# Kernel tuning notes

Measured on AMD Instinct MI355X. Metric: run time of the kernel, lower is better.

Reference implementation:

```python
import jax, jax.numpy as jnp
import numpy as np

NUM_HEADS = 32
NUM_KV_HEADS = 8
HEAD_DIM = 128
SCALE = 0.08838834764831845  # 1/sqrt(HEAD_DIM)
SEQ_LEN = 2048
NEG_INF = -1e30


def setup_inputs() -> dict:
    key = jax.random.key(0)
    k1, k2, k3 = jax.random.split(key, 3)
    query = jax.random.normal(k1, (SEQ_LEN, NUM_HEADS * HEAD_DIM), dtype=jnp.float32)
    key_t = jax.random.normal(k2, (SEQ_LEN, NUM_KV_HEADS * HEAD_DIM), dtype=jnp.float32)
    value = jax.random.normal(k3, (SEQ_LEN, NUM_KV_HEADS * HEAD_DIM), dtype=jnp.float32)
    return {"query": query, "key": key_t, "value": value}


def reference(query, key, value):
    S = query.shape[0]
    n_rep = NUM_HEADS // NUM_KV_HEADS
    # GQA: group q heads by kv head instead of materializing repeated K/V.
    q = query.reshape(S, NUM_KV_HEADS, n_rep, HEAD_DIM)   # [S, G, R, D]
    k = key.reshape(S, NUM_KV_HEADS, HEAD_DIM)            # [S, G, D]
    v = value.reshape(S, NUM_KV_HEADS, HEAD_DIM)          # [S, G, D]
    # scores: [G, R, S(query), S(key)]
    scores = jnp.einsum('sgrd,tgd->grst', q, k) * jnp.float32(SCALE)
    # causal mask (prefill: seq_len > 1 -> is_causal=True)
    causal = jnp.arange(S)[:, None] >= jnp.arange(S)[None, :]  # [S, S]
    scores = jnp.where(causal, scores, NEG_INF)
    probs = jax.nn.softmax(scores, axis=-1)
    out = jnp.einsum('grst,tgd->sgrd', probs, v)          # [S, G, R, D]
    return out.reshape(S, NUM_HEADS * HEAD_DIM)
```

## Files before the change

kernel.cpp:

```cpp
#include <hip/hip_runtime.h>


#define SEQ    2048
#define NH     32
#define NKV    8
#define DHEAD  128
#define QROW   (NH * DHEAD)
#define KVROW  (NKV * DHEAD)
#define SCALE  0.08838834764831845f
#define LOG2E  1.4426950408889634f
#define BN     64
#define VSTRP  132

typedef __attribute__((ext_vector_type(8))) short bf16x8;
typedef __attribute__((ext_vector_type(8))) unsigned short u16x8;
typedef __attribute__((ext_vector_type(16))) float f32x16;
typedef __attribute__((ext_vector_type(4))) unsigned int u32x4;

static __device__ __forceinline__ unsigned short f2bf(float f) {
  unsigned int u = __float_as_uint(f);
  return (unsigned short)((u + 0x7fffu + ((u >> 16) & 1u)) >> 16);
}

static __device__ __forceinline__ unsigned cvtpk_bf16(float lo, float hi) {
  unsigned r;
  asm("v_cvt_pk_bf16_f32 %0, %1, %2" : "=v"(r) : "v"(lo), "v"(hi));
  return r;
}

static __device__ __forceinline__ f32x16 zero16() {
  f32x16 z;
#pragma unroll
  for (int i = 0; i < 16; ++i) z[i] = 0.f;
  return z;
}

__global__ __launch_bounds__(256) void prep_kernel(
    const float* __restrict__ K, const float* __restrict__ V,
    unsigned short* __restrict__ Kg, unsigned short* __restrict__ VTg) {
  __shared__ unsigned short Vs[16 * VSTRP];
  const int t0  = blockIdx.x * 16;
  const int g   = blockIdx.y;
  const int tid = threadIdx.x;
#pragma unroll
  for (int e = 0; e < 2; ++e) {
    int fi = e * 256 + tid;
    int t  = fi >> 5;
    int c4 = fi & 31;
    const float4 kv = *(const float4*)(K + (size_t)(t0 + t) * KVROW + g * DHEAD + c4 * 4);
    ushort4 kb4 = {f2bf(kv.x), f2bf(kv.y), f2bf(kv.z), f2bf(kv.w)};
    *(ushort4*)(Kg + ((size_t)(g * SEQ + t0 + t) << 7) + c4 * 4) = kb4;
    const float4 vv = *(const float4*)(V + (size_t)(t0 + t) * KVROW + g * DHEAD + c4 * 4);
    ushort4 vb4 = {f2bf(vv.x), f2bf(vv.y), f2bf(vv.z), f2bf(vv.w)};
    *(ushort4*)&Vs[t * VSTRP + c4 * 4] = vb4;
  }
  __syncthreads();
  {
    int d  = tid >> 1;
    int tb = tid & 1;
    u16x8 o;
#pragma unroll
    for (int j = 0; j < 8; ++j) o[j] = Vs[(tb * 8 + j) * VSTRP + d];
    *(u16x8*)(VTg + (size_t)(g * DHEAD + d) * SEQ + t0 + tb * 8) = o;
  }
}

static __device__ __forceinline__ void stage_kv(
    const unsigned short* __restrict__ Kg, const unsigned short* __restrict__ VTg,
    unsigned short* kbuf, unsigned short* vbuf, int g, int kt, int w, int lane) {
  const int t0 = kt * BN;
#pragma unroll
  for (int c = 0; c < 4; ++c) {
    int off = (w * 4 + c) * 512 + lane * 8;
    int tl  = off >> 7;
    int dsw = (off & 127) ^ (8 * (tl & 15));
    const unsigned short* src = Kg + ((size_t)(g * SEQ + t0 + tl) << 7) + dsw;
    __builtin_amdgcn_global_load_lds(
        (const __attribute__((address_space(1))) void*)src,
        (__attribute__((address_space(3))) void*)(kbuf + (w * 4 + c) * 512), 16, 0, 0);
  }
#pragma unroll
  for (int c = 0; c < 4; ++c) {
    int off = (w * 4 + c) * 512 + lane * 8;
    int dl  = off >> 6;
    int tsw = (off & 63) ^ (8 * (dl & 7));
    const unsigned short* src = VTg + (size_t)(g * DHEAD + dl) * SEQ + t0 + tsw;
    __builtin_amdgcn_global_load_lds(
        (const __attribute__((address_space(1))) void*)src,
        (__attribute__((address_space(3))) void*)(vbuf + (w * 4 + c) * 512), 16, 0, 0);
  }
}

#define PV_KSTEP(PP, S, KS2)                                                     \
  do {                                                                           \
    unsigned y0 = cvtpk_bf16((PP)[(2 * (S)) * 4 + 0], (PP)[(2 * (S)) * 4 + 1]);  \
    unsigned z0 = cvtpk_bf16((PP)[(2 * (S)) * 4 + 2], (PP)[(2 * (S)) * 4 + 3]);  \
    unsigned y1 = cvtpk_bf16((PP)[(2 * (S) + 1) * 4 + 0], (PP)[(2 * (S) + 1) * 4 + 1]); \
    unsigned z1 = cvtpk_bf16((PP)[(2 * (S) + 1) * 4 + 2], (PP)[(2 * (S) + 1) * 4 + 3]); \
    asm("v_permlane32_swap_b32 %0, %1" : "+v"(y0), "+v"(y1));                    \
    asm("v_permlane32_swap_b32 %0, %1" : "+v"(z0), "+v"(z1));                    \
    u32x4 paw = (u32x4){y0, z0, y1, z1};                                         \
    bf16x8 pa = __builtin_bit_cast(bf16x8, paw);                                 \
    const int tcol = (KS2) * 16 + hi * 8;                                        \
    _Pragma("unroll")                                                            \
    for (int nd = 0; nd < 4; ++nd) {                                             \
      int drow = nd * 32 + l32;                                                  \
      bf16x8 vf = *(const bf16x8*)&Vb[cur][drow * BN + (tcol ^ (8 * (drow & 7)))]; \
      oacc[nd] = __builtin_amdgcn_mfma_f32_32x32x16_bf16(pa, vf, oacc[nd], 0, 0, 0); \
    }                                                                            \
  } while (0)

__global__ __launch_bounds__(256, 2) void sdpa_w32_kernel(
    const float* __restrict__ Q, float* __restrict__ O,
    const unsigned short* __restrict__ Kg, const unsigned short* __restrict__ VTg) {
  __shared__ unsigned short Kb[2][BN * DHEAD];
  __shared__ unsigned short Vb[2][DHEAD * BN];
  __shared__ float Ls[4][32];

  const int b   = blockIdx.x;
  const int g   = b & 7;
  const int q5  = (b >> 3) & 31;
  const int jj  = (b >= 256) ? q5 : 63 - q5;
  const int q0  = jj * 32;
  const int nt  = (jj >> 1) + 1;
  const int tid = threadIdx.x;
  const int w   = tid >> 6;
  const int lane = tid & 63;
  const int l32 = lane & 31;
  const int hi  = lane >> 5;
  const int h   = g * 4 + w;

  bf16x8 qf[8];
  {
    const float* qp = Q + (size_t)(q0 + l32) * QROW + h * DHEAD + hi * 8;
#pragma unroll
    for (int ks = 0; ks < 8; ++ks) {
      const float4 a = *(const float4*)(qp + ks * 16);
      const float4 c = *(const float4*)(qp + ks * 16 + 4);
      bf16x8 v;
      v[0] = (short)f2bf(a.x * (SCALE * LOG2E));
      v[1] = (short)f2bf(a.y * (SCALE * LOG2E));
      v[2] = (short)f2bf(a.z * (SCALE * LOG2E));
      v[3] = (short)f2bf(a.w * (SCALE * LOG2E));
      v[4] = (short)f2bf(c.x * (SCALE * LOG2E));
      v[5] = (short)f2bf(c.y * (SCALE * LOG2E));
      v[6] = (short)f2bf(c.z * (SCALE * LOG2E));
      v[7] = (short)f2bf(c.w * (SCALE * LOG2E));
      qf[ks] = v;
    }
  }

  f32x16 oacc[4];
#pragma unroll
  for (int i = 0; i < 4; ++i) oacc[i] = zero16();
  float lsum = 0.f;

  stage_kv(Kg, VTg, Kb[0], Vb[0], g, 0, w, lane);
  __syncthreads();

  for (int kt = 0; kt < nt; ++kt) {
    const int cur = kt & 1;
    if (kt + 1 < nt)
      stage_kv(Kg, VTg, Kb[cur ^ 1], Vb[cur ^ 1], g, kt + 1, w, lane);

    const bool diag = (kt == nt - 1);
    const int KB = (diag && !(jj & 1)) ? 1 : 2;

    f32x16 s0 = zero16();
    f32x16 s1 = zero16();
#pragma unroll
    for (int ks = 0; ks < 8; ++ks) {
      const int t = l32;
      bf16x8 kf = *(const bf16x8*)&Kb[cur][t * DHEAD + (((ks * 16 + hi * 8)) ^ (8 * (t & 15)))];
      s0 = __builtin_amdgcn_mfma_f32_32x32x16_bf16(kf, qf[ks], s0, 0, 0, 0);
    }
    if (KB == 2) {
#pragma unroll
      for (int ks = 0; ks < 8; ++ks) {
        const int t = 32 + l32;
        bf16x8 kf = *(const bf16x8*)&Kb[cur][t * DHEAD + (((ks * 16 + hi * 8)) ^ (8 * (t & 15)))];
        s1 = __builtin_amdgcn_mfma_f32_32x32x16_bf16(kf, qf[ks], s1, 0, 0, 0);
      }
    }

    const int keyb = kt * BN;
    f32x16 p0, p1;
#pragma unroll
    for (int r = 0; r < 16; ++r) {
      const int ko = (r & 3) + 8 * (r >> 2) + 4 * hi;
      float x = s0[r];
      x = (diag && (keyb + ko > q0 + l32)) ? -1e30f : x;
      float e = __builtin_amdgcn_exp2f(x);
      p0[r] = e;
      lsum += e;
    }
    if (KB == 2) {
#pragma unroll
      for (int r = 0; r < 16; ++r) {
        const int ko = 32 + (r & 3) + 8 * (r >> 2) + 4 * hi;
        float x = s1[r];
        x = (diag && (keyb + ko > q0 + l32)) ? -1e30f : x;
        float e = __builtin_amdgcn_exp2f(x);
        p1[r] = e;
        lsum += e;
      }
    }

    PV_KSTEP(p0, 0, 0);
    PV_KSTEP(p0, 1, 1);
    if (KB == 2) {
      PV_KSTEP(p1, 0, 2);
      PV_KSTEP(p1, 1, 3);
    }

    __syncthreads();
  }

  {
    float tot = lsum + __shfl_xor(lsum, 32);
    if (hi == 0) Ls[w][l32] = 1.f / tot;
  }
  __syncthreads();
#pragma unroll
  for (int nd = 0; nd < 4; ++nd) {
#pragma unroll
    for (int r = 0; r < 16; ++r) {
      const int row = (r & 3) + 8 * (r >> 2) + 4 * hi;
      O[(size_t)(q0 + row) * QROW + h * DHEAD + nd * 32 + l32] = oacc[nd][r] * Ls[w][row];
    }
  }
}

extern "C" void kernel_launch(void* const* d_in, const int* in_sizes, int n_in,
                              void* d_out, int out_size, void* d_ws, size_t ws_size,
                              hipStream_t stream) {
  (void)in_sizes; (void)n_in; (void)out_size; (void)ws_size;
  const float* Q = (const float*)d_in[0];
  const float* K = (const float*)d_in[1];
  const float* V = (const float*)d_in[2];
  float* O = (float*)d_out;
  unsigned short* Kg  = (unsigned short*)d_ws;
  unsigned short* VTg = Kg + (size_t)NKV * SEQ * DHEAD;
  prep_kernel<<<dim3(SEQ / 16, NKV), 256, 0, stream>>>(K, V, Kg, VTg);
  sdpa_w32_kernel<<<512, 256, 0, stream>>>(Q, O, Kg, VTg);
}
```

Baseline: 153.0 us.

## Split key tiles across waves and read K/V directly from global memory

Each block now handles a single query head, and its four waves take interleaved key tiles, a split-K layout. The double-buffered LDS staging of K and V is replaced by direct global (cache) loads. Per-wave partial outputs and row sums are combined in shared memory with atomic adds before the final normalisation. This raises the block count and drops the per-tile barriers, at the cost of uncoalesced global fragment loads, four times as many redundant K/V reads across heads, and LDS atomic reductions.

```diff
diff --git a/kernel.cpp b/kernel.cpp
--- a/kernel.cpp
+++ b/kernel.cpp
@@ -65,32 +65,6 @@
   }
 }
 
-static __device__ __forceinline__ void stage_kv(
-    const unsigned short* __restrict__ Kg, const unsigned short* __restrict__ VTg,
-    unsigned short* kbuf, unsigned short* vbuf, int g, int kt, int w, int lane) {
-  const int t0 = kt * BN;
-#pragma unroll
-  for (int c = 0; c < 4; ++c) {
-    int off = (w * 4 + c) * 512 + lane * 8;
-    int tl  = off >> 7;
-    int dsw = (off & 127) ^ (8 * (tl & 15));
-    const unsigned short* src = Kg + ((size_t)(g * SEQ + t0 + tl) << 7) + dsw;
-    __builtin_amdgcn_global_load_lds(
-        (const __attribute__((address_space(1))) void*)src,
-        (__attribute__((address_space(3))) void*)(kbuf + (w * 4 + c) * 512), 16, 0, 0);
-  }
-#pragma unroll
-  for (int c = 0; c < 4; ++c) {
-    int off = (w * 4 + c) * 512 + lane * 8;
-    int dl  = off >> 6;
-    int tsw = (off & 63) ^ (8 * (dl & 7));
-    const unsigned short* src = VTg + (size_t)(g * DHEAD + dl) * SEQ + t0 + tsw;
-    __builtin_amdgcn_global_load_lds(
-        (const __attribute__((address_space(1))) void*)src,
-        (__attribute__((address_space(3))) void*)(vbuf + (w * 4 + c) * 512), 16, 0, 0);
-  }
-}
-
 #define PV_KSTEP(PP, S, KS2)                                                     \
   do {                                                                           \
     unsigned y0 = cvtpk_bf16((PP)[(2 * (S)) * 4 + 0], (PP)[(2 * (S)) * 4 + 1]);  \
@@ -101,34 +75,33 @@
     asm("v_permlane32_swap_b32 %0, %1" : "+v"(z0), "+v"(z1));                    \
     u32x4 paw = (u32x4){y0, z0, y1, z1};                                         \
     bf16x8 pa = __builtin_bit_cast(bf16x8, paw);                                 \
-    const int tcol = (KS2) * 16 + hi * 8;                                        \
+    const int tcol = keyb + (KS2) * 16 + hi * 8;                                 \
     _Pragma("unroll")                                                            \
     for (int nd = 0; nd < 4; ++nd) {                                             \
-      int drow = nd * 32 + l32;                                                  \
-      bf16x8 vf = *(const bf16x8*)&Vb[cur][drow * BN + (tcol ^ (8 * (drow & 7)))]; \
+      bf16x8 vf = *(const bf16x8*)(Vbase + (nd * 32 + l32) * SEQ + tcol);        \
       oacc[nd] = __builtin_amdgcn_mfma_f32_32x32x16_bf16(pa, vf, oacc[nd], 0, 0, 0); \
     }                                                                            \
   } while (0)
 
-__global__ __launch_bounds__(256, 2) void sdpa_w32_kernel(
+__global__ __launch_bounds__(256, 3) void sdpa_nolds_kernel(
     const float* __restrict__ Q, float* __restrict__ O,
     const unsigned short* __restrict__ Kg, const unsigned short* __restrict__ VTg) {
-  __shared__ unsigned short Kb[2][BN * DHEAD];
-  __shared__ unsigned short Vb[2][DHEAD * BN];
-  __shared__ float Ls[4][32];
-
-  const int b   = blockIdx.x;
-  const int g   = b & 7;
-  const int q5  = (b >> 3) & 31;
-  const int jj  = (b >= 256) ? q5 : 63 - q5;
-  const int q0  = jj * 32;
-  const int nt  = (jj >> 1) + 1;
-  const int tid = threadIdx.x;
-  const int w   = tid >> 6;
+  __shared__ float Obuf[32 * 128];
+  __shared__ float Lbuf[32];
+
+  const int b      = blockIdx.x;
+  const int g      = b & 7;
+  const int hh     = (b >> 3) & 3;
+  const int jjcode = b >> 5;
+  const int jj     = 63 - jjcode;
+  const int q0     = jj * 32;
+  const int nt     = (jj >> 1) + 1;
+  const int tid  = threadIdx.x;
+  const int s    = tid >> 6;
   const int lane = tid & 63;
-  const int l32 = lane & 31;
-  const int hi  = lane >> 5;
-  const int h   = g * 4 + w;
+  const int l32  = lane & 31;
+  const int hi   = lane >> 5;
+  const int h    = g * 4 + hh;
 
   bf16x8 qf[8];
   {
@@ -155,35 +128,30 @@
   for (int i = 0; i < 4; ++i) oacc[i] = zero16();
   float lsum = 0.f;
 
-  stage_kv(Kg, VTg, Kb[0], Vb[0], g, 0, w, lane);
-  __syncthreads();
-
-  for (int kt = 0; kt < nt; ++kt) {
-    const int cur = kt & 1;
-    if (kt + 1 < nt)
-      stage_kv(Kg, VTg, Kb[cur ^ 1], Vb[cur ^ 1], g, kt + 1, w, lane);
-
+  const unsigned short* Kbase = Kg + ((size_t)(g * SEQ) << 7);
+  const unsigned short* Vbase = VTg + (size_t)(g * DHEAD) * SEQ;
+
+  for (int kt = s; kt < nt; kt += 4) {
+    const int keyb = kt * BN;
     const bool diag = (kt == nt - 1);
     const int KB = (diag && !(jj & 1)) ? 1 : 2;
 
+    const unsigned short* kp = Kbase + ((keyb + l32) << 7) + hi * 8;
     f32x16 s0 = zero16();
     f32x16 s1 = zero16();
 #pragma unroll
     for (int ks = 0; ks < 8; ++ks) {
-      const int t = l32;
-      bf16x8 kf = *(const bf16x8*)&Kb[cur][t * DHEAD + (((ks * 16 + hi * 8)) ^ (8 * (t & 15)))];
+      bf16x8 kf = *(const bf16x8*)(kp + ks * 16);
       s0 = __builtin_amdgcn_mfma_f32_32x32x16_bf16(kf, qf[ks], s0, 0, 0, 0);
     }
     if (KB == 2) {
 #pragma unroll
       for (int ks = 0; ks < 8; ++ks) {
-        const int t = 32 + l32;
-        bf16x8 kf = *(const bf16x8*)&Kb[cur][t * DHEAD + (((ks * 16 + hi * 8)) ^ (8 * (t & 15)))];
+        bf16x8 kf = *(const bf16x8*)(kp + 32 * DHEAD + ks * 16);
         s1 = __builtin_amdgcn_mfma_f32_32x32x16_bf16(kf, qf[ks], s1, 0, 0, 0);
       }
     }
 
-    const int keyb = kt * BN;
     f32x16 p0, p1;
 #pragma unroll
     for (int r = 0; r < 16; ++r) {
@@ -212,21 +180,35 @@
       PV_KSTEP(p1, 0, 2);
       PV_KSTEP(p1, 1, 3);
     }
-
-    __syncthreads();
-  }
-
+  }
+
+  for (int i = tid; i < 32 * 128; i += 256) Obuf[i] = 0.f;
+  if (tid < 32) Lbuf[tid] = 0.f;
+  __syncthreads();
   {
     float tot = lsum + __shfl_xor(lsum, 32);
-    if (hi == 0) Ls[w][l32] = 1.f / tot;
-  }
-  __syncthreads();
-#pragma unroll
-  for (int nd = 0; nd < 4; ++nd) {
+    if (hi == 0) atomicAdd(&Lbuf[l32], tot);
+  }
+#pragma unroll
+  for (int nd = 0; nd < 4; ++nd)
 #pragma unroll
     for (int r = 0; r < 16; ++r) {
       const int row = (r & 3) + 8 * (r >> 2) + 4 * hi;
-      O[(size_t)(q0 + row) * QROW + h * DHEAD + nd * 32 + l32] = oacc[nd][r] * Ls[w][row];
+      atomicAdd(&Obuf[row * 128 + nd * 32 + l32], oacc[nd][r]);
+    }
+  __syncthreads();
+
+  {
+    const int row = tid >> 3;
+    const int c0  = (tid & 7) * 16;
+    const float inv = 1.f / Lbuf[row];
+    float* orow = O + (size_t)(q0 + row) * QROW + h * DHEAD + c0;
+    const float* src = &Obuf[row * 128 + c0];
+#pragma unroll
+    for (int j = 0; j < 4; ++j) {
+      float4 v = *(const float4*)(src + j * 4);
+      v.x *= inv; v.y *= inv; v.z *= inv; v.w *= inv;
+      *(float4*)(orow + j * 4) = v;
     }
   }
 }
@@ -242,5 +224,5 @@
   unsigned short* Kg  = (unsigned short*)d_ws;
   unsigned short* VTg = Kg + (size_t)NKV * SEQ * DHEAD;
   prep_kernel<<<dim3(SEQ / 16, NKV), 256, 0, stream>>>(K, V, Kg, VTg);
-  sdpa_w32_kernel<<<512, 256, 0, stream>>>(Q, O, Kg, VTg);
-}
+  sdpa_nolds_kernel<<<2048, 256, 0, stream>>>(Q, O, Kg, VTg);
+}
```

Result: slower. 333.6 us (+118.0%).

## Pair light and heavy query tiles per block with shared KV ring and split-K merge

Applied to the files above, without the earlier changes.

Replaces the 512-block, 4-wave kernel with 256 blocks of 8 waves. Each block pairs a short causal query tile with its mirrored long one and streams the shared K/V tiles through a 4-deep LDS ring. One wave group finishes the light tile, then both groups split the remaining key tiles of the heavy tile and merge partial outputs and sums through LDS. It also raises wave priority around the MFMA sections. The aim is to balance causal work, reuse each staged KV tile across both query tiles, and hide load latency with deeper prefetch, at the cost of more LDS, a merge step and more complex control flow.

```diff
diff --git a/kernel.cpp b/kernel.cpp
--- a/kernel.cpp
+++ b/kernel.cpp
@@ -65,29 +65,49 @@
   }
 }
 
-static __device__ __forceinline__ void stage_kv(
+static __device__ __forceinline__ void stage_tile(
     const unsigned short* __restrict__ Kg, const unsigned short* __restrict__ VTg,
-    unsigned short* kbuf, unsigned short* vbuf, int g, int kt, int w, int lane) {
-  const int t0 = kt * BN;
-#pragma unroll
-  for (int c = 0; c < 4; ++c) {
-    int off = (w * 4 + c) * 512 + lane * 8;
+    unsigned short* kbuf, unsigned short* vbuf, int g, int t, int w, int lane) {
+  const int t0 = t * BN;
+#pragma unroll
+  for (int c = 0; c < 2; ++c) {
+    int off = (w * 2 + c) * 512 + lane * 8;
     int tl  = off >> 7;
     int dsw = (off & 127) ^ (8 * (tl & 15));
     const unsigned short* src = Kg + ((size_t)(g * SEQ + t0 + tl) << 7) + dsw;
     __builtin_amdgcn_global_load_lds(
         (const __attribute__((address_space(1))) void*)src,
-        (__attribute__((address_space(3))) void*)(kbuf + (w * 4 + c) * 512), 16, 0, 0);
-  }
-#pragma unroll
-  for (int c = 0; c < 4; ++c) {
-    int off = (w * 4 + c) * 512 + lane * 8;
+        (__attribute__((address_space(3))) void*)(kbuf + (w * 2 + c) * 512), 16, 0, 0);
+  }
+#pragma unroll
+  for (int c = 0; c < 2; ++c) {
+    int off = (w * 2 + c) * 512 + lane * 8;
     int dl  = off >> 6;
     int tsw = (off & 63) ^ (8 * (dl & 7));
     const unsigned short* src = VTg + (size_t)(g * DHEAD + dl) * SEQ + t0 + tsw;
     __builtin_amdgcn_global_load_lds(
         (const __attribute__((address_space(1))) void*)src,
-        (__attribute__((address_space(3))) void*)(vbuf + (w * 4 + c) * 512), 16, 0, 0);
+        (__attribute__((address_space(3))) void*)(vbuf + (w * 2 + c) * 512), 16, 0, 0);
+  }
+}
+
+static __device__ __forceinline__ void load_qf(
+    const float* __restrict__ Q, int q0, int h, int l32, int hi, bf16x8* qf) {
+  const float* qp = Q + (size_t)(q0 + l32) * QROW + h * DHEAD + hi * 8;
+#pragma unroll
+  for (int ks = 0; ks < 8; ++ks) {
+    const float4 a = *(const float4*)(qp + ks * 16);
+    const float4 c = *(const float4*)(qp + ks * 16 + 4);
+    bf16x8 v;
+    v[0] = (short)f2bf(a.x * (SCALE * LOG2E));
+    v[1] = (short)f2bf(a.y * (SCALE * LOG2E));
+    v[2] = (short)f2bf(a.z * (SCALE * LOG2E));
+    v[3] = (short)f2bf(a.w * (SCALE * LOG2E));
+    v[4] = (short)f2bf(c.x * (SCALE * LOG2E));
+    v[5] = (short)f2bf(c.y * (SCALE * LOG2E));
+    v[6] = (short)f2bf(c.z * (SCALE * LOG2E));
+    v[7] = (short)f2bf(c.w * (SCALE * LOG2E));
+    qf[ks] = v;
   }
 }
 
@@ -105,128 +125,177 @@
     _Pragma("unroll")                                                            \
     for (int nd = 0; nd < 4; ++nd) {                                             \
       int drow = nd * 32 + l32;                                                  \
-      bf16x8 vf = *(const bf16x8*)&Vb[cur][drow * BN + (tcol ^ (8 * (drow & 7)))]; \
+      bf16x8 vf = *(const bf16x8*)&vb[drow * BN + (tcol ^ (8 * (drow & 7)))];    \
       oacc[nd] = __builtin_amdgcn_mfma_f32_32x32x16_bf16(pa, vf, oacc[nd], 0, 0, 0); \
     }                                                                            \
   } while (0)
 
-__global__ __launch_bounds__(256, 2) void sdpa_w32_kernel(
+static __device__ __forceinline__ void compute_tile(
+    const unsigned short* kb, const unsigned short* vb,
+    const bf16x8* qf, f32x16* oacc, float& lsum,
+    int keyb, int q0, bool diag, int KB, int l32, int hi) {
+  f32x16 s0 = zero16();
+  f32x16 s1 = zero16();
+  __builtin_amdgcn_s_setprio(1);
+#pragma unroll
+  for (int ks = 0; ks < 8; ++ks) {
+    const int t = l32;
+    bf16x8 kf = *(const bf16x8*)&kb[t * DHEAD + ((ks * 16 + hi * 8) ^ (8 * (t & 15)))];
+    s0 = __builtin_amdgcn_mfma_f32_32x32x16_bf16(kf, qf[ks], s0, 0, 0, 0);
+  }
+  if (KB == 2) {
+#pragma unroll
+    for (int ks = 0; ks < 8; ++ks) {
+      const int t = 32 + l32;
+      bf16x8 kf = *(const bf16x8*)&kb[t * DHEAD + ((ks * 16 + hi * 8) ^ (8 * (t & 15)))];
+      s1 = __builtin_amdgcn_mfma_f32_32x32x16_bf16(kf, qf[ks], s1, 0, 0, 0);
+    }
+  }
+  __builtin_amdgcn_s_setprio(0);
+
+  f32x16 p0, p1;
+#pragma unroll
+  for (int r = 0; r < 16; ++r) {
+    const int ko = (r & 3) + 8 * (r >> 2) + 4 * hi;
+    float x = s0[r];
+    x = (diag && (keyb + ko > q0 + l32)) ? -1e30f : x;
+    float e = __builtin_amdgcn_exp2f(x);
+    p0[r] = e;
+    lsum += e;
+  }
+  if (KB == 2) {
+#pragma unroll
+    for (int r = 0; r < 16; ++r) {
+      const int ko = 32 + (r & 3) + 8 * (r >> 2) + 4 * hi;
+      float x = s1[r];
+      x = (diag && (keyb + ko > q0 + l32)) ? -1e30f : x;
+      float e = __builtin_amdgcn_exp2f(x);
+      p1[r] = e;
+      lsum += e;
+    }
+  }
+
+  __builtin_amdgcn_s_setprio(1);
+  PV_KSTEP(p0, 0, 0);
+  PV_KSTEP(p0, 1, 1);
+  if (KB == 2) {
+    PV_KSTEP(p1, 0, 2);
+    PV_KSTEP(p1, 1, 3);
+  }
+  __builtin_amdgcn_s_setprio(0);
+}
+
+__global__ __launch_bounds__(512, 2) void sdpa_pair_kernel(
     const float* __restrict__ Q, float* __restrict__ O,
     const unsigned short* __restrict__ Kg, const unsigned short* __restrict__ VTg) {
-  __shared__ unsigned short Kb[2][BN * DHEAD];
-  __shared__ unsigned short Vb[2][DHEAD * BN];
-  __shared__ float Ls[4][32];
-
-  const int b   = blockIdx.x;
-  const int g   = b & 7;
-  const int q5  = (b >> 3) & 31;
-  const int jj  = (b >= 256) ? q5 : 63 - q5;
-  const int q0  = jj * 32;
-  const int nt  = (jj >> 1) + 1;
-  const int tid = threadIdx.x;
-  const int w   = tid >> 6;
+  __shared__ unsigned short Kring[4][BN * DHEAD];
+  __shared__ unsigned short Vring[4][DHEAD * BN];
+  __shared__ float Lb[4][32];
+
+  const int b  = blockIdx.x;
+  const int g  = b & 7;
+  const int p  = b >> 3;
+  const int nt_l = (p + 2) >> 1;
+  const int nt_h = 33 - nt_l;
+  const int jj_h = 63 - p;
+  const int tid  = threadIdx.x;
+  const int w    = tid >> 6;
   const int lane = tid & 63;
-  const int l32 = lane & 31;
-  const int hi  = lane >> 5;
-  const int h   = g * 4 + w;
+  const int l32  = lane & 31;
+  const int hi   = lane >> 5;
+  const int grp  = w >> 2;
+  const int wg   = w & 3;
+  const int h    = g * 4 + wg;
+
+  const int myjj_l = p;
+  int q0 = (grp ? p : jj_h) * 32;
 
   bf16x8 qf[8];
-  {
-    const float* qp = Q + (size_t)(q0 + l32) * QROW + h * DHEAD + hi * 8;
-#pragma unroll
-    for (int ks = 0; ks < 8; ++ks) {
-      const float4 a = *(const float4*)(qp + ks * 16);
-      const float4 c = *(const float4*)(qp + ks * 16 + 4);
-      bf16x8 v;
-      v[0] = (short)f2bf(a.x * (SCALE * LOG2E));
-      v[1] = (short)f2bf(a.y * (SCALE * LOG2E));
-      v[2] = (short)f2bf(a.z * (SCALE * LOG2E));
-      v[3] = (short)f2bf(a.w * (SCALE * LOG2E));
-      v[4] = (short)f2bf(c.x * (SCALE * LOG2E));
-      v[5] = (short)f2bf(c.y * (SCALE * LOG2E));
-      v[6] = (short)f2bf(c.z * (SCALE * LOG2E));
-      v[7] = (short)f2bf(c.w * (SCALE * LOG2E));
-      qf[ks] = v;
-    }
-  }
+  load_qf(Q, q0, h, l32, hi, qf);
 
   f32x16 oacc[4];
 #pragma unroll
   for (int i = 0; i < 4; ++i) oacc[i] = zero16();
   float lsum = 0.f;
 
-  stage_kv(Kg, VTg, Kb[0], Vb[0], g, 0, w, lane);
+#pragma unroll
+  for (int t = 0; t < 4; ++t)
+    stage_tile(Kg, VTg, Kring[t], Vring[t], g, t, w, lane);
   __syncthreads();
 
-  for (int kt = 0; kt < nt; ++kt) {
-    const int cur = kt & 1;
-    if (kt + 1 < nt)
-      stage_kv(Kg, VTg, Kb[cur ^ 1], Vb[cur ^ 1], g, kt + 1, w, lane);
-
-    const bool diag = (kt == nt - 1);
-    const int KB = (diag && !(jj & 1)) ? 1 : 2;
-
-    f32x16 s0 = zero16();
-    f32x16 s1 = zero16();
-#pragma unroll
-    for (int ks = 0; ks < 8; ++ks) {
-      const int t = l32;
-      bf16x8 kf = *(const bf16x8*)&Kb[cur][t * DHEAD + (((ks * 16 + hi * 8)) ^ (8 * (t & 15)))];
-      s0 = __builtin_amdgcn_mfma_f32_32x32x16_bf16(kf, qf[ks], s0, 0, 0, 0);
-    }
-    if (KB == 2) {
-#pragma unroll
-      for (int ks = 0; ks < 8; ++ks) {
-        const int t = 32 + l32;
-        bf16x8 kf = *(const bf16x8*)&Kb[cur][t * DHEAD + (((ks * 16 + hi * 8)) ^ (8 * (t & 15)))];
-        s1 = __builtin_amdgcn_mfma_f32_32x32x16_bf16(kf, qf[ks], s1, 0, 0, 0);
+  int ct = 0, sn = 4;
+  for (int it = 0; it < 17; ++it) {
+    int nc;
+    if (it < nt_l) {
+      const int t = it;
+      const bool diag = (grp == 1) && (t == nt_l - 1);
+      const int KB = (diag && !(myjj_l & 1)) ? 1 : 2;
+      compute_tile(Kring[t & 3], Vring[t & 3], qf, oacc, lsum,
+                   t * BN, q0, diag, KB, l32, hi);
+      nc = 1;
+      if (grp == 1 && t == nt_l - 1) {
+        float tot = lsum + __shfl_xor(lsum, 32);
+        float inv = 1.f / tot;
+#pragma unroll
+        for (int nd = 0; nd < 4; ++nd)
+#pragma unroll
+          for (int r = 0; r < 16; ++r) {
+            const int row = (r & 3) + 8 * (r >> 2) + 4 * hi;
+            O[(size_t)(q0 + row) * QROW + h * DHEAD + nd * 32 + l32] =
+                oacc[nd][r] * __shfl(inv, row);
+          }
+#pragma unroll
+        for (int i = 0; i < 4; ++i) oacc[i] = zero16();
+        lsum = 0.f;
+        q0 = jj_h * 32;
+        load_qf(Q, q0, h, l32, hi, qf);
       }
-    }
-
-    const int keyb = kt * BN;
-    f32x16 p0, p1;
-#pragma unroll
-    for (int r = 0; r < 16; ++r) {
-      const int ko = (r & 3) + 8 * (r >> 2) + 4 * hi;
-      float x = s0[r];
-      x = (diag && (keyb + ko > q0 + l32)) ? -1e30f : x;
-      float e = __builtin_amdgcn_exp2f(x);
-      p0[r] = e;
-      lsum += e;
-    }
-    if (KB == 2) {
-#pragma unroll
-      for (int r = 0; r < 16; ++r) {
-        const int ko = 32 + (r & 3) + 8 * (r >> 2) + 4 * hi;
-        float x = s1[r];
-        x = (diag && (keyb + ko > q0 + l32)) ? -1e30f : x;
-        float e = __builtin_amdgcn_exp2f(x);
-        p1[r] = e;
-        lsum += e;
+    } else {
+      const int j  = it - nt_l;
+      const int tA = nt_l + 2 * j;
+      const int t  = tA + grp;
+      if (t < nt_h) {
+        const bool diag = (t == nt_h - 1);
+        const int KB = (diag && !(jj_h & 1)) ? 1 : 2;
+        compute_tile(Kring[t & 3], Vring[t & 3], qf, oacc, lsum,
+                     t * BN, q0, diag, KB, l32, hi);
       }
-    }
-
-    PV_KSTEP(p0, 0, 0);
-    PV_KSTEP(p0, 1, 1);
-    if (KB == 2) {
-      PV_KSTEP(p1, 0, 2);
-      PV_KSTEP(p1, 1, 3);
-    }
-
+      nc = (tA + 1 < nt_h) ? 2 : 1;
+    }
+    ct += nc;
     __syncthreads();
-  }
-
+    for (int k2 = 0; k2 < nc && sn < nt_h; ++k2, ++sn)
+      stage_tile(Kg, VTg, Kring[sn & 3], Vring[sn & 3], g, sn, w, lane);
+  }
+
+  float* OvF = (float*)&Kring[0][0];
   {
     float tot = lsum + __shfl_xor(lsum, 32);
-    if (hi == 0) Ls[w][l32] = 1.f / tot;
-  }
-  __syncthreads();
-#pragma unroll
-  for (int nd = 0; nd < 4; ++nd) {
-#pragma unroll
-    for (int r = 0; r < 16; ++r) {
-      const int row = (r & 3) + 8 * (r >> 2) + 4 * hi;
-      O[(size_t)(q0 + row) * QROW + h * DHEAD + nd * 32 + l32] = oacc[nd][r] * Ls[w][row];
+    if (grp == 1) {
+      if (hi == 0) Lb[wg][l32] = tot;
+      float* ob = OvF + wg * (32 * 128);
+#pragma unroll
+      for (int nd = 0; nd < 4; ++nd)
+#pragma unroll
+        for (int r = 0; r < 16; ++r) {
+          const int row = (r & 3) + 8 * (r >> 2) + 4 * hi;
+          ob[row * 128 + nd * 32 + l32] = oacc[nd][r];
+        }
+    }
+    __syncthreads();
+    if (grp == 0) {
+      tot += Lb[wg][l32];
+      float inv = 1.f / tot;
+      const float* ob = OvF + wg * (32 * 128);
+#pragma unroll
+      for (int nd = 0; nd < 4; ++nd)
+#pragma unroll
+        for (int r = 0; r < 16; ++r) {
+          const int row = (r & 3) + 8 * (r >> 2) + 4 * hi;
+          float val = oacc[nd][r] + ob[row * 128 + nd * 32 + l32];
+          O[(size_t)(q0 + row) * QROW + h * DHEAD + nd * 32 + l32] =
+              val * __shfl(inv, row);
+        }
     }
   }
 }
@@ -242,5 +311,5 @@
   unsigned short* Kg  = (unsigned short*)d_ws;
   unsigned short* VTg = Kg + (size_t)NKV * SEQ * DHEAD;
   prep_kernel<<<dim3(SEQ / 16, NKV), 256, 0, stream>>>(K, V, Kg, VTg);
-  sdpa_w32_kernel<<<512, 256, 0, stream>>>(Q, O, Kg, VTg);
-}
+  sdpa_pair_kernel<<<256, 512, 0, stream>>>(Q, O, Kg, VTg);
+}
```

Result: faster. 144.0 us (-5.9%).
